# Kernel tuning notes

Measured on AMD Instinct MI355X. Metric: run time of the kernel, lower is better.

Reference implementation:

```python
import jax, jax.numpy as jnp
import numpy as np

B, C, F, G = 256, 4096, 64, 512   # batch, candidates, features, max taxi groups per sample
H1, H2 = 128, 128                 # scorer hidden dims
HB = 32                           # taxi bias net hidden dim
NEG = -1e9


def setup_inputs() -> dict:
    key = jax.random.key(0)
    ks = jax.random.split(key, 8)
    feats = jax.random.normal(ks[0], (B, C, F), jnp.float32)
    gids = jax.random.randint(ks[1], (B, C), -1, G)            # -1 = defer
    mask = (jax.random.uniform(ks[2], (B, C)) < 0.9).astype(jnp.float32)
    x_with_meta = jnp.concatenate(
        [feats, gids.astype(jnp.float32)[..., None], mask[..., None]], axis=-1)

    def lin(k, i, o):
        return (jax.random.normal(k, (i, o), jnp.float32) / np.sqrt(i)).astype(jnp.float32)

    return {
        "x_with_meta": x_with_meta,
        "W0": lin(ks[3], F, H1),  "b0": jnp.zeros((H1,), jnp.float32),
        "W1": lin(ks[4], H1, H2), "b1": jnp.zeros((H2,), jnp.float32),
        "W2": lin(ks[5], H2, 1),  "b2": jnp.zeros((1,), jnp.float32),
        "Wb0": lin(ks[6], 3, HB), "bb0": jnp.zeros((HB,), jnp.float32),
        "Wb1": lin(ks[7], HB, 1), "bb1": jnp.zeros((1,), jnp.float32),
    }


def _forward(x_with_meta, W0, b0, W1, b1, W2, b2, Wb0, bb0, Wb1, bb1):
    mask = x_with_meta[..., -1]                     # [B, C]
    gids = x_with_meta[..., -2].astype(jnp.int32)   # [B, C], -1 = defer
    feats = x_with_meta[..., :-2]                   # [B, C, F]

    # CandidateScorerMLP (dropout is identity at inference)
    h = jax.nn.relu(feats @ W0 + b0)
    h = jax.nn.relu(h @ W1 + b1)
    raw = (h @ W2 + b2)[..., 0]                     # [B, C]
    raw = jnp.where(mask > 0.0, raw, NEG)

    valid = (mask > 0.0) & (gids >= 0)              # [B, C]
    nseg = B * G + 1                                # +1 dummy segment for invalid/defer
    seg = jnp.where(valid, jnp.arange(B, dtype=jnp.int32)[:, None] * G + gids, B * G)
    segf = seg.reshape(-1)
    validf = valid.reshape(-1)
    rawf = raw.reshape(-1)

    cnt = jax.ops.segment_sum(validf.astype(jnp.float32), segf, num_segments=nseg)
    ssum = jax.ops.segment_sum(jnp.where(validf, rawf, 0.0), segf, num_segments=nseg)
    smax = jax.ops.segment_max(jnp.where(validf, rawf, NEG), segf, num_segments=nseg)
    smax = jnp.where(cnt > 0.0, smax, 0.0)          # sanitize empty segments
    mean = ssum / jnp.maximum(cnt, 1.0)
    multi = cnt > 1.0                               # normalization only for group size > 1

    # Per-group taxi quality bias from pooled stats [max, mean, size]
    stats = jnp.where(multi[:, None], jnp.stack([smax, mean, cnt], axis=-1), 0.0)  # [nseg, 3]
    bias = (jax.nn.relu(stats @ Wb0 + bb0) @ Wb1 + bb1)[:, 0]                      # [nseg]

    mean_c = mean[segf].reshape(B, C)
    max_c = smax[segf].reshape(B, C)
    bias_c = bias[segf].reshape(B, C)
    apply = valid & multi[segf].reshape(B, C)

    # raw - mean + max - 0.5*(max - raw) + bias  ==  1.5*raw - mean + 0.5*max + bias
    fair = jnp.where(apply, 1.5 * raw - mean_c + 0.5 * max_c + bias_c, raw)
    fair = jnp.where(mask > 0.0, fair, NEG)
    return fair, mask


def reference(x_with_meta, W0, b0, W1, b1, W2, b2, Wb0, bb0, Wb1, bb1):
    return _forward(x_with_meta, W0, b0, W1, b1, W2, b2, Wb0, bb0, Wb1, bb1)
```

## Files before the change

kernel.cpp:

```cpp
#include <hip/hip_runtime.h>
#include <hip/hip_bf16.h>

#define NB   256
#define NC   4096
#define NG   512
#define NH   128
#define NELEM (NB*NC)
#define LDX  66
#define NEGV (-1000000000.0f)
#define TILES 16
#define TILE_ROWS 128
#define GRID_MLP (NELEM/(TILES*TILE_ROWS))

typedef __attribute__((ext_vector_type(8))) short short8;
typedef __attribute__((ext_vector_type(4))) float f32x4;

__device__ __forceinline__ unsigned pack2(float x, float y) {
    return (__float_as_uint(y) & 0xFFFF0000u) | (__float_as_uint(x) >> 16);
}
__device__ __forceinline__ unsigned short f2bf(float f) {
    unsigned u = __float_as_uint(f);
    return (unsigned short)((u + 0x7FFFu + ((u >> 16) & 1u)) >> 16);
}
__device__ __forceinline__ unsigned char f2fp8(float f) {
    return (unsigned char)((unsigned)__builtin_amdgcn_cvt_pk_fp8_f32(f, 0.f, 0, false) & 0xFFu);
}
__device__ __forceinline__ unsigned encf(float f) {
    unsigned u = __float_as_uint(f);
    return (u & 0x80000000u) ? ~u : (u | 0x80000000u);
}
__device__ __forceinline__ float decf(unsigned u) {
    unsigned v = (u & 0x80000000u) ? (u ^ 0x80000000u) : ~u;
    return __uint_as_float(v);
}
__device__ __forceinline__ f32x4 mfma_bf16(short8 a, short8 b, f32x4 c) {
    return __builtin_amdgcn_mfma_f32_16x16x32_bf16(a, b, c, 0, 0, 0);
}
__device__ __forceinline__ f32x4 mfma_fp8(long a, long b, f32x4 c) {
    return __builtin_amdgcn_mfma_f32_16x16x32_fp8_fp8(a, b, c, 0, 0, 0);
}

__device__ __forceinline__ void gload16(const float* g, float* lds) {
    __builtin_amdgcn_global_load_lds(
        (const __attribute__((address_space(1))) void*)g,
        (__attribute__((address_space(3))) void*)lds,
        16, 0, 0);
}

__global__ void k_prep(const float* __restrict__ W0, const float* __restrict__ W1,
                       unsigned short* __restrict__ W0T, unsigned char* __restrict__ W1f8s) {
    int i = blockIdx.x * 256 + threadIdx.x;
    if (i < 8192) {
        int j = i >> 6, k = i & 63;
        W0T[i] = f2bf(W0[k * NH + j]);
    } else if (i < 24576) {
        int i2 = i - 8192;
        int j = i2 >> 7, c = i2 & 127;
        W1f8s[(j * 16 + ((c >> 3) ^ (j & 7))) * 8 + (c & 7)] = f2fp8(W1[c * NH + j]);
    }
}

__global__ __launch_bounds__(256, 2) void k_mlp(
        const float* __restrict__ X,
        const unsigned short* __restrict__ W0T,
        const unsigned char* __restrict__ W1f8s,
        const float* __restrict__ b0, const float* __restrict__ b1,
        const float* __restrict__ W2, const float* __restrict__ b2p,
        float* __restrict__ rawOut, unsigned* __restrict__ mcodeOut) {
    __shared__ __align__(16) unsigned char sW1f[16384];
    __shared__ __align__(16) float sFeat[4][2048];
    __shared__ __align__(16) unsigned char sHs[4][4096];
    __shared__ float sB0[128];
    __shared__ float sB1W2[256];

    const int t = threadIdx.x, w = t >> 6, l = t & 63;
    const int l15 = l & 15, g = l >> 4;
    const int rx = l15 & 7;

    {
        const uint4* src = (const uint4*)W1f8s;
        uint4* dst = (uint4*)sW1f;
#pragma unroll
        for (int i = 0; i < 4; ++i) dst[i * 256 + t] = src[i * 256 + t];
    }
    if (t < 128) { sB0[t] = b0[t]; sB1W2[t] = b1[t]; sB1W2[128 + t] = W2[t]; }

    short8 w0f[8][2];
#pragma unroll
    for (int n = 0; n < 8; ++n)
#pragma unroll
        for (int kk = 0; kk < 2; ++kk)
            w0f[n][kk] = *(const short8*)(W0T + (n * 16 + l15) * 64 + kk * 32 + g * 8);
    const float b2v = b2p[0];

    __syncthreads();

    float* fw = sFeat[w];
    unsigned char* hs = sHs[w];
    const size_t rowwave0 = (size_t)blockIdx.x * (TILES * TILE_ROWS) + w * 32;

    const int r4 = l >> 4, sl = l & 15;
    const int offE = r4 * LDX + ((sl ^ r4) << 2);
    const int offO = r4 * LDX + ((sl ^ (r4 + 4)) << 2);

    {
        const float* gb = X + rowwave0 * LDX;
#pragma unroll
        for (int k = 0; k < 8; ++k)
            gload16(gb + k * 4 * LDX + ((k & 1) ? offO : offE), fw + k * 256);
    }
    float2 mt = make_float2(0.f, 0.f), mtN = make_float2(0.f, 0.f);
    if (l < 32) mt = *(const float2*)(X + (rowwave0 + l) * LDX + 64);

    for (int tau = 0; tau < TILES; ++tau) {
        const size_t rowb = rowwave0 + (size_t)tau * TILE_ROWS;

        if (tau == 0) asm volatile("s_waitcnt vmcnt(0)" ::: "memory");
        else         asm volatile("s_waitcnt vmcnt(3)" ::: "memory");
        __builtin_amdgcn_sched_barrier(0);

        short8 bfr[2][2];
#pragma unroll
        for (int rg = 0; rg < 2; ++rg)
#pragma unroll
            for (int kk = 0; kk < 2; ++kk) {
                const int row = rg * 16 + l15;
                const int u0 = kk * 8 + 2 * g;
                const float* base = fw + row * 64;
                float4 fa = *(const float4*)(base + ((u0 ^ rx) << 2));
                float4 fb = *(const float4*)(base + (((u0 + 1) ^ rx) << 2));
                union { unsigned u[4]; short8 s; } tu;
                tu.u[0] = pack2(fa.x, fa.y); tu.u[1] = pack2(fa.z, fa.w);
                tu.u[2] = pack2(fb.x, fb.y); tu.u[3] = pack2(fb.z, fb.w);
                bfr[rg][kk] = tu.s;
            }

        asm volatile("s_waitcnt lgkmcnt(0)" ::: "memory");
        __builtin_amdgcn_sched_barrier(0);
        if (tau + 1 < TILES) {
            const float* gb = X + (rowb + TILE_ROWS) * LDX;
#pragma unroll
            for (int k = 0; k < 8; ++k)
                gload16(gb + k * 4 * LDX + ((k & 1) ? offO : offE), fw + k * 256);
            if (l < 32) mtN = *(const float2*)(X + (rowb + TILE_ROWS + l) * LDX + 64);
        }
        __builtin_amdgcn_sched_barrier(0);

#pragma unroll
        for (int nh = 0; nh < 2; ++nh) {
            f32x4 acc[4][2];
#pragma unroll
            for (int n4 = 0; n4 < 4; ++n4)
#pragma unroll
                for (int rg = 0; rg < 2; ++rg) acc[n4][rg] = (f32x4){0.f, 0.f, 0.f, 0.f};
#pragma unroll
            for (int n4 = 0; n4 < 4; ++n4) {
                const int n = nh * 4 + n4;
#pragma unroll
                for (int rg = 0; rg < 2; ++rg) {
                    acc[n4][rg] = mfma_bf16(w0f[n][0], bfr[rg][0], acc[n4][rg]);
                    acc[n4][rg] = mfma_bf16(w0f[n][1], bfr[rg][1], acc[n4][rg]);
                }
            }
#pragma unroll
            for (int n4 = 0; n4 < 4; ++n4) {
                const int n = nh * 4 + n4;
                const int c0 = n * 16 + g * 4;
                const float bv0 = sB0[c0], bv1 = sB0[c0+1], bv2 = sB0[c0+2], bv3 = sB0[c0+3];
                const int u = (2 * n + (g >> 1)) ^ rx;
#pragma unroll
                for (int rg = 0; rg < 2; ++rg) {
                    unsigned d0 = (unsigned)__builtin_amdgcn_cvt_pk_fp8_f32(
                        fmaxf(acc[n4][rg][0] + bv0, 0.f), fmaxf(acc[n4][rg][1] + bv1, 0.f), 0, false);
                    d0 = (unsigned)__builtin_amdgcn_cvt_pk_fp8_f32(
                        fmaxf(acc[n4][rg][2] + bv2, 0.f), fmaxf(acc[n4][rg][3] + bv3, 0.f), (int)d0, true);
                    *(unsigned*)(hs + ((rg * 16 + l15) * 16 + u) * 8 + (g & 1) * 4) = d0;
                }
            }
        }

        asm volatile("" ::: "memory");

        long a2[2][4];
#pragma unroll
        for (int rg = 0; rg < 2; ++rg)
#pragma unroll
            for (int kk = 0; kk < 4; ++kk)
                a2[rg][kk] = *(const long*)(hs + ((rg * 16 + l15) * 16 + ((kk * 4 + g) ^ rx)) * 8);

        float rq[2][4] = {{0.f,0.f,0.f,0.f},{0.f,0.f,0.f,0.f}};
#pragma unroll
        for (int n = 0; n < 8; ++n) {
            f32x4 acc2[2] = {(f32x4){0.f,0.f,0.f,0.f}, (f32x4){0.f,0.f,0.f,0.f}};
            const unsigned char* wrow = sW1f + (n * 16 + l15) * 128;
#pragma unroll
            for (int kk = 0; kk < 4; ++kk) {
                long bb = *(const long*)(wrow + ((kk * 4 + g) ^ rx) * 8);
                acc2[0] = mfma_fp8(a2[0][kk], bb, acc2[0]);
                acc2[1] = mfma_fp8(a2[1][kk], bb, acc2[1]);
            }
            const float b1v = sB1W2[n * 16 + l15], w2v = sB1W2[128 + n * 16 + l15];
#pragma unroll
            for (int rg = 0; rg < 2; ++rg)
#pragma unroll
                for (int q = 0; q < 4; ++q)
                    rq[rg][q] += fmaxf(acc2[rg][q] + b1v, 0.f) * w2v;
        }

#pragma unroll
        for (int off = 1; off < 16; off <<= 1)
#pragma unroll
            for (int rg = 0; rg < 2; ++rg)
#pragma unroll
                for (int q = 0; q < 4; ++q)
                    rq[rg][q] += __shfl_xor(rq[rg][q], off, 64);
        if (l15 == 0) {
#pragma unroll
            for (int rg = 0; rg < 2; ++rg) {
                const size_t m0 = rowb + rg * 16 + g * 4;
                *(float4*)(rawOut + m0) = make_float4(rq[rg][0] + b2v, rq[rg][1] + b2v,
                                                      rq[rg][2] + b2v, rq[rg][3] + b2v);
            }
        }
        if (l < 32) {
            const unsigned pmcu = ((unsigned)((int)mt.x + 1) << 1) | (mt.y > 0.f ? 1u : 0u);
            mcodeOut[rowb + l] = pmcu;
        }
        mt = mtN;
    }
}

__global__ __launch_bounds__(256) void k_bstats(
        const float* __restrict__ raw, const unsigned* __restrict__ mcode,
        const float* __restrict__ Wb0, const float* __restrict__ bb0,
        const float* __restrict__ Wb1, const float* __restrict__ bb1,
        float* __restrict__ out) {
    __shared__ unsigned scnt[512];
    __shared__ float    ssum[512];
    __shared__ unsigned smx[512];
    __shared__ float4   sstat[512];
    const int b = blockIdx.x, t = threadIdx.x;
    scnt[t] = 0u; ssum[t] = 0.f; smx[t] = 0u;
    scnt[t + 256] = 0u; ssum[t + 256] = 0.f; smx[t + 256] = 0u;
    __syncthreads();
    const int base = b * NC;
#pragma unroll 4
    for (int it = 0; it < 16; ++it) {
        int m = base + it * 256 + t;
        unsigned c = mcode[m];
        if ((c & 1u) && (c >> 1)) {
            int s = (int)(c >> 1) - 1;
            float r = raw[m];
            atomicAdd(&scnt[s], 1u);
            atomicAdd(&ssum[s], r);
            atomicMax(&smx[s], encf(r));
        }
    }
    __syncthreads();
#pragma unroll
    for (int k = 0; k < 2; ++k) {
        int s = t + k * 256;
        unsigned c = scnt[s];
        float smax = (c > 0) ? decf(smx[s]) : 0.f;
        float mean = ssum[s] / fmaxf((float)c, 1.f);
        float multi = (c > 1) ? 1.f : 0.f;
        float bias = 0.f;
        if (c > 1) {
            bias = bb1[0];
#pragma unroll
            for (int j = 0; j < 32; ++j) {
                float h = smax * Wb0[j] + mean * Wb0[32 + j] + (float)c * Wb0[64 + j] + bb0[j];
                bias += fmaxf(h, 0.f) * Wb1[j];
            }
        }
        sstat[s] = make_float4(smax, mean, bias, multi);
    }
    __syncthreads();
    const float4* raw4 = (const float4*)raw;
    const uint4*  mc4  = (const uint4*)mcode;
#pragma unroll
    for (int it = 0; it < 4; ++it) {
        int i = b * 1024 + it * 256 + t;
        float4 rv = raw4[i];
        uint4 mc = mc4[i];
        const float r[4]    = {rv.x, rv.y, rv.z, rv.w};
        const unsigned m[4] = {mc.x, mc.y, mc.z, mc.w};
        float fair[4], msk[4];
#pragma unroll
        for (int j = 0; j < 4; ++j) {
            msk[j] = (m[j] & 1u) ? 1.0f : 0.0f;
            float f;
            if (m[j] & 1u) {
                f = r[j];
                if (m[j] >> 1) {
                    float4 st = sstat[(int)(m[j] >> 1) - 1];
                    if (st.w > 0.5f) f = 1.5f * r[j] - st.y + 0.5f * st.x + st.z;
                }
            } else {
                f = NEGV;
            }
            fair[j] = f;
        }
        const size_t m0 = (size_t)i * 4;
        *(float4*)(out + m0) = make_float4(fair[0], fair[1], fair[2], fair[3]);
        *(float4*)(out + NELEM + m0) = make_float4(msk[0], msk[1], msk[2], msk[3]);
    }
}

extern "C" void kernel_launch(void* const* d_in, const int* in_sizes, int n_in,
                              void* d_out, int out_size, void* d_ws, size_t ws_size,
                              hipStream_t stream) {
    const float* X   = (const float*)d_in[0];
    const float* W0  = (const float*)d_in[1];
    const float* b0  = (const float*)d_in[2];
    const float* W1  = (const float*)d_in[3];
    const float* b1  = (const float*)d_in[4];
    const float* W2  = (const float*)d_in[5];
    const float* b2  = (const float*)d_in[6];
    const float* Wb0 = (const float*)d_in[7];
    const float* bb0 = (const float*)d_in[8];
    const float* Wb1 = (const float*)d_in[9];
    const float* bb1 = (const float*)d_in[10];

    char* ws = (char*)d_ws;
    float*          raw      = (float*)(ws + 0);
    unsigned*       mcode    = (unsigned*)(ws + 4194304);
    unsigned short* W0T      = (unsigned short*)(ws + 8388608);
    unsigned char*  W1f8s    = (unsigned char*)(ws + 8404992);

    k_prep<<<96, 256, 0, stream>>>(W0, W1, W0T, W1f8s);
    k_mlp<<<GRID_MLP, 256, 0, stream>>>(X, W0T, W1f8s, b0, b1, W2, b2, raw, mcode);
    k_bstats<<<NB, 256, 0, stream>>>(raw, mcode, Wb0, bb0, Wb1, bb1, (float*)d_out);
}
```

Before: 91.36 us.

## Fuse scorer MLP and group-stats pass into one per-batch kernel

The MLP kernel and the segment-statistics/output kernel are merged into one kernel with one 512-thread block per batch row. Raw scores and the mask/group codes now stay in shared memory instead of going out to a global workspace and being read back, and one kernel launch goes away. The per-group epilogue is also folded into a single precomputed delta (0.5*max - mean + bias) plus a multi flag. The cost is a much larger shared-memory footprint, likely only one block per CU, and a simpler full vmcnt wait in the load loop.

```diff
diff --git a/kernel.cpp b/kernel.cpp
--- a/kernel.cpp
+++ b/kernel.cpp
@@ -9,8 +9,6 @@
 #define LDX  66
 #define NEGV (-1000000000.0f)
 #define TILES 16
-#define TILE_ROWS 128
-#define GRID_MLP (NELEM/(TILES*TILE_ROWS))
 
 typedef __attribute__((ext_vector_type(8))) short short8;
 typedef __attribute__((ext_vector_type(4))) float f32x4;
@@ -60,30 +58,40 @@
     }
 }
 
-__global__ __launch_bounds__(256, 2) void k_mlp(
+__global__ __launch_bounds__(512, 2) void k_fused(
         const float* __restrict__ X,
         const unsigned short* __restrict__ W0T,
         const unsigned char* __restrict__ W1f8s,
         const float* __restrict__ b0, const float* __restrict__ b1,
         const float* __restrict__ W2, const float* __restrict__ b2p,
-        float* __restrict__ rawOut, unsigned* __restrict__ mcodeOut) {
+        const float* __restrict__ Wb0, const float* __restrict__ bb0,
+        const float* __restrict__ Wb1, const float* __restrict__ bb1,
+        float* __restrict__ out) {
     __shared__ __align__(16) unsigned char sW1f[16384];
-    __shared__ __align__(16) float sFeat[4][2048];
-    __shared__ __align__(16) unsigned char sHs[4][4096];
+    __shared__ __align__(16) float sFeat[8][2048];
+    __shared__ __align__(16) unsigned char sHs[8][4096];
     __shared__ float sB0[128];
     __shared__ float sB1W2[256];
+    __shared__ __align__(16) float sraw[4096];
+    __shared__ unsigned short smc[4096];
+    __shared__ unsigned scnt[512];
+    __shared__ float    ssum[512];
+    __shared__ unsigned smx[512];
+    __shared__ float    sdelta[512];
+    __shared__ unsigned char smulti[512];
 
     const int t = threadIdx.x, w = t >> 6, l = t & 63;
     const int l15 = l & 15, g = l >> 4;
     const int rx = l15 & 7;
+    const int b = blockIdx.x;
 
     {
         const uint4* src = (const uint4*)W1f8s;
         uint4* dst = (uint4*)sW1f;
-#pragma unroll
-        for (int i = 0; i < 4; ++i) dst[i * 256 + t] = src[i * 256 + t];
+        dst[t] = src[t]; dst[512 + t] = src[512 + t];
     }
     if (t < 128) { sB0[t] = b0[t]; sB1W2[t] = b1[t]; sB1W2[128 + t] = W2[t]; }
+    scnt[t] = 0u; ssum[t] = 0.f; smx[t] = 0u;
 
     short8 w0f[8][2];
 #pragma unroll
@@ -97,7 +105,8 @@
 
     float* fw = sFeat[w];
     unsigned char* hs = sHs[w];
-    const size_t rowwave0 = (size_t)blockIdx.x * (TILES * TILE_ROWS) + w * 32;
+    const size_t rowwave0 = (size_t)b * NC + w * 32;
+    const int lrow0 = w * 32;
 
     const int r4 = l >> 4, sl = l & 15;
     const int offE = r4 * LDX + ((sl ^ r4) << 2);
@@ -113,10 +122,10 @@
     if (l < 32) mt = *(const float2*)(X + (rowwave0 + l) * LDX + 64);
 
     for (int tau = 0; tau < TILES; ++tau) {
-        const size_t rowb = rowwave0 + (size_t)tau * TILE_ROWS;
-
-        if (tau == 0) asm volatile("s_waitcnt vmcnt(0)" ::: "memory");
-        else         asm volatile("s_waitcnt vmcnt(3)" ::: "memory");
+        const size_t rowb = rowwave0 + (size_t)tau * 256;
+        const int lrow = lrow0 + tau * 256;
+
+        asm volatile("s_waitcnt vmcnt(0)" ::: "memory");
         __builtin_amdgcn_sched_barrier(0);
 
         short8 bfr[2][2];
@@ -138,11 +147,11 @@
         asm volatile("s_waitcnt lgkmcnt(0)" ::: "memory");
         __builtin_amdgcn_sched_barrier(0);
         if (tau + 1 < TILES) {
-            const float* gb = X + (rowb + TILE_ROWS) * LDX;
+            const float* gb = X + (rowb + 256) * LDX;
 #pragma unroll
             for (int k = 0; k < 8; ++k)
                 gload16(gb + k * 4 * LDX + ((k & 1) ? offO : offE), fw + k * 256);
-            if (l < 32) mtN = *(const float2*)(X + (rowb + TILE_ROWS + l) * LDX + 64);
+            if (l < 32) mtN = *(const float2*)(X + (rowb + 256 + l) * LDX + 64);
         }
         __builtin_amdgcn_sched_barrier(0);
 
@@ -217,93 +226,79 @@
         if (l15 == 0) {
 #pragma unroll
             for (int rg = 0; rg < 2; ++rg) {
-                const size_t m0 = rowb + rg * 16 + g * 4;
-                *(float4*)(rawOut + m0) = make_float4(rq[rg][0] + b2v, rq[rg][1] + b2v,
-                                                      rq[rg][2] + b2v, rq[rg][3] + b2v);
+                const int lm0 = lrow + rg * 16 + g * 4;
+                *(float4*)(sraw + lm0) = make_float4(rq[rg][0] + b2v, rq[rg][1] + b2v,
+                                                     rq[rg][2] + b2v, rq[rg][3] + b2v);
             }
         }
         if (l < 32) {
             const unsigned pmcu = ((unsigned)((int)mt.x + 1) << 1) | (mt.y > 0.f ? 1u : 0u);
-            mcodeOut[rowb + l] = pmcu;
+            smc[lrow + l] = (unsigned short)pmcu;
         }
         mt = mtN;
     }
-}
-
-__global__ __launch_bounds__(256) void k_bstats(
-        const float* __restrict__ raw, const unsigned* __restrict__ mcode,
-        const float* __restrict__ Wb0, const float* __restrict__ bb0,
-        const float* __restrict__ Wb1, const float* __restrict__ bb1,
-        float* __restrict__ out) {
-    __shared__ unsigned scnt[512];
-    __shared__ float    ssum[512];
-    __shared__ unsigned smx[512];
-    __shared__ float4   sstat[512];
-    const int b = blockIdx.x, t = threadIdx.x;
-    scnt[t] = 0u; ssum[t] = 0.f; smx[t] = 0u;
-    scnt[t + 256] = 0u; ssum[t + 256] = 0.f; smx[t + 256] = 0u;
+
     __syncthreads();
-    const int base = b * NC;
-#pragma unroll 4
-    for (int it = 0; it < 16; ++it) {
-        int m = base + it * 256 + t;
-        unsigned c = mcode[m];
+
+#pragma unroll
+    for (int it = 0; it < 8; ++it) {
+        int m = it * 512 + t;
+        unsigned c = smc[m];
         if ((c & 1u) && (c >> 1)) {
             int s = (int)(c >> 1) - 1;
-            float r = raw[m];
+            float r = sraw[m];
             atomicAdd(&scnt[s], 1u);
             atomicAdd(&ssum[s], r);
             atomicMax(&smx[s], encf(r));
         }
     }
     __syncthreads();
-#pragma unroll
-    for (int k = 0; k < 2; ++k) {
-        int s = t + k * 256;
-        unsigned c = scnt[s];
-        float smax = (c > 0) ? decf(smx[s]) : 0.f;
-        float mean = ssum[s] / fmaxf((float)c, 1.f);
-        float multi = (c > 1) ? 1.f : 0.f;
-        float bias = 0.f;
+
+    {
+        unsigned c = scnt[t];
+        float delta = 0.f; unsigned char multi = 0;
         if (c > 1) {
-            bias = bb1[0];
+            float smaxv = decf(smx[t]);
+            float mean = ssum[t] / (float)c;
+            float bias = bb1[0];
 #pragma unroll
             for (int j = 0; j < 32; ++j) {
-                float h = smax * Wb0[j] + mean * Wb0[32 + j] + (float)c * Wb0[64 + j] + bb0[j];
+                float h = smaxv * Wb0[j] + mean * Wb0[32 + j] + (float)c * Wb0[64 + j] + bb0[j];
                 bias += fmaxf(h, 0.f) * Wb1[j];
             }
-        }
-        sstat[s] = make_float4(smax, mean, bias, multi);
+            delta = 0.5f * smaxv - mean + bias;
+            multi = 1;
+        }
+        sdelta[t] = delta; smulti[t] = multi;
     }
     __syncthreads();
-    const float4* raw4 = (const float4*)raw;
-    const uint4*  mc4  = (const uint4*)mcode;
-#pragma unroll
-    for (int it = 0; it < 4; ++it) {
-        int i = b * 1024 + it * 256 + t;
-        float4 rv = raw4[i];
-        uint4 mc = mc4[i];
-        const float r[4]    = {rv.x, rv.y, rv.z, rv.w};
-        const unsigned m[4] = {mc.x, mc.y, mc.z, mc.w};
+
+    const size_t gbase = (size_t)b * NC;
+#pragma unroll
+    for (int it = 0; it < 2; ++it) {
+        int i = it * 512 + t;
+        int m0 = i * 4;
+        float4 rv = *(const float4*)(sraw + m0);
+        const float r[4] = {rv.x, rv.y, rv.z, rv.w};
         float fair[4], msk[4];
 #pragma unroll
         for (int j = 0; j < 4; ++j) {
-            msk[j] = (m[j] & 1u) ? 1.0f : 0.0f;
+            unsigned c = smc[m0 + j];
+            msk[j] = (c & 1u) ? 1.0f : 0.0f;
             float f;
-            if (m[j] & 1u) {
+            if (c & 1u) {
                 f = r[j];
-                if (m[j] >> 1) {
-                    float4 st = sstat[(int)(m[j] >> 1) - 1];
-                    if (st.w > 0.5f) f = 1.5f * r[j] - st.y + 0.5f * st.x + st.z;
+                if (c >> 1) {
+                    int s = (int)(c >> 1) - 1;
+                    if (smulti[s]) f = 1.5f * r[j] + sdelta[s];
                 }
             } else {
                 f = NEGV;
             }
             fair[j] = f;
         }
-        const size_t m0 = (size_t)i * 4;
-        *(float4*)(out + m0) = make_float4(fair[0], fair[1], fair[2], fair[3]);
-        *(float4*)(out + NELEM + m0) = make_float4(msk[0], msk[1], msk[2], msk[3]);
+        *(float4*)(out + gbase + m0) = make_float4(fair[0], fair[1], fair[2], fair[3]);
+        *(float4*)(out + NELEM + gbase + m0) = make_float4(msk[0], msk[1], msk[2], msk[3]);
     }
 }
 
@@ -323,12 +318,10 @@
     const float* bb1 = (const float*)d_in[10];
 
     char* ws = (char*)d_ws;
-    float*          raw      = (float*)(ws + 0);
-    unsigned*       mcode    = (unsigned*)(ws + 4194304);
-    unsigned short* W0T      = (unsigned short*)(ws + 8388608);
-    unsigned char*  W1f8s    = (unsigned char*)(ws + 8404992);
+    unsigned short* W0T   = (unsigned short*)(ws + 0);
+    unsigned char*  W1f8s = (unsigned char*)(ws + 16384);
 
     k_prep<<<96, 256, 0, stream>>>(W0, W1, W0T, W1f8s);
-    k_mlp<<<GRID_MLP, 256, 0, stream>>>(X, W0T, W1f8s, b0, b1, W2, b2, raw, mcode);
-    k_bstats<<<NB, 256, 0, stream>>>(raw, mcode, Wb0, bb0, Wb1, bb1, (float*)d_out);
-}
+    k_fused<<<NB, 512, 0, stream>>>(X, W0T, W1f8s, b0, b1, W2, b2,
+                                    Wb0, bb0, Wb1, bb1, (float*)d_out);
+}
```

New measurement: 81.35 us. 11.0% less time.
